# Performance work log

Hardware: AMD Instinct MI355X
Metric: run time of the kernel (lower is better)

## Reference

```python
import jax, jax.numpy as jnp
import numpy as np

K_SIZE = 5  # kernel_size


def _patches(f, k):
    # f: (b, c, h, w) -> (b, c, k*k, h, w), matching torch.nn.Unfold ordering
    # (patch positions row-major (kh, kw) per channel), padding = k//2, stride 1.
    p = k // 2
    b, c, h, w = f.shape
    fp = jnp.pad(f, ((0, 0), (0, 0), (p, p), (p, p)))
    slices = [fp[:, :, i:i + h, j:j + w] for i in range(k) for j in range(k)]
    return jnp.stack(slices, axis=2)


def _conv1x1(w, b, f):
    # w: (out, in), b: (out,), f: (b, in, h, w)
    return jnp.einsum('oc,bchw->bohw', w, f) + b[None, :, None, None]


def setup_inputs() -> dict:
    key = jax.random.key(0)
    ks = jax.random.split(key, 8)
    B, XC, YC, FT, H, W = 4, 64, 64, 64, 128, 128
    x = jax.random.normal(ks[0], (B, XC, H, W), dtype=jnp.float32)
    y = jax.random.normal(ks[1], (B, YC, H, W), dtype=jnp.float32)
    sx = 1.0 / np.sqrt(XC)
    sy = 1.0 / np.sqrt(YC)
    sf = 1.0 / np.sqrt(FT)
    wx = jax.random.uniform(ks[2], (FT, XC), jnp.float32, -sx, sx)
    bx = jax.random.uniform(ks[3], (FT,), jnp.float32, -sx, sx)
    wy = jax.random.uniform(ks[4], (FT, YC), jnp.float32, -sy, sy)
    by = jax.random.uniform(ks[5], (FT,), jnp.float32, -sy, sy)
    wo = jax.random.uniform(ks[6], (XC, FT), jnp.float32, -sf, sf)
    bo = jax.random.uniform(ks[7], (XC,), jnp.float32, -sf, sf)
    return {"x": x, "y": y, "wx": wx, "bx": bx, "wy": wy, "by": by, "wo": wo, "bo": bo}


def reference(x, y, wx, bx, wy, by, wo, bo):
    k = K_SIZE
    q = _conv1x1(wy, by, y)            # (b, feat, h, w): Q (the q axis of size 1 is squeezed)
    Kp = _patches(q, k)                # (b, feat, k^2, h, w): unfold(conv_y(y))
    v = _conv1x1(wx, bx, x)            # (b, feat, h, w)
    Vp = _patches(v, k)                # (b, feat, k^2, h, w): unfold(conv_x(x))
    A = jnp.einsum('bckhw,bchw->bkhw', Kp, q)   # scores over k^2 neighbors
    A = jax.nn.softmax(A, axis=1)               # softmax over dim=1 (k^2)
    out = jnp.einsum('bkhw,bckhw->bchw', A, Vp)  # aggregate values
    out = _conv1x1(wo, bo, out)
    return out + x
```

## Files before the change

### kernel.cpp

```cpp
#include <hip/hip_runtime.h>

#define HH   128
#define WW   128
#define HW   (HH * WW)
#define CC   64
#define BB   4
#define TILE 8
#define HALO 12

typedef unsigned int uint32;
typedef _Float16 h2  __attribute__((ext_vector_type(2)));
typedef __fp16   h2b __attribute__((ext_vector_type(2)));

__device__ __forceinline__ uint32 pkrtz(float a, float b) {
    h2b r = __builtin_amdgcn_cvt_pkrtz(a, b);
    return __builtin_bit_cast(uint32, r);
}
__device__ __forceinline__ float dot2(uint32 a, uint32 b, float c) {
#if __has_builtin(__builtin_amdgcn_fdot2)
    return __builtin_amdgcn_fdot2(__builtin_bit_cast(h2b, a),
                                  __builtin_bit_cast(h2b, b), c, false);
#else
    h2 x = __builtin_bit_cast(h2, a), y = __builtin_bit_cast(h2, b);
    return c + (float)x.x * (float)y.x + (float)x.y * (float)y.y;
#endif
}

__global__ __launch_bounds__(256, 4)
void qv_kernel(const float* __restrict__ x, const float* __restrict__ y,
               const float* __restrict__ wx, const float* __restrict__ bx,
               const float* __restrict__ wy, const float* __restrict__ by,
               uint32* __restrict__ qws, uint32* __restrict__ vws)
{
    __shared__ uint32 yP[32 * 64];
    __shared__ uint32 xP[32 * 64];
    __shared__ uint32 wyP[32 * 64];
    __shared__ uint32 wxP[32 * 64];

    const int t  = threadIdx.x;
    const int w0 = blockIdx.x * 64;
    const int h  = blockIdx.y;
    const int b  = blockIdx.z;

    {
        const int px = t & 63;
        const size_t rb = (size_t)b * CC * HW + (size_t)h * WW + w0 + px;
        #pragma unroll
        for (int i = 0; i < 8; ++i) {
            const int icp = (t >> 6) * 8 + i;
            const float y0 = y[rb + (size_t)(2 * icp) * HW];
            const float y1 = y[rb + (size_t)(2 * icp + 1) * HW];
            const float x0 = x[rb + (size_t)(2 * icp) * HW];
            const float x1 = x[rb + (size_t)(2 * icp + 1) * HW];
            yP[icp * 64 + px] = pkrtz(y0, y1);
            xP[icp * 64 + px] = pkrtz(x0, x1);
        }
        const int oc = t & 63;
        #pragma unroll
        for (int i = 0; i < 8; ++i) {
            const int icp = (t >> 6) * 8 + i;
            wyP[icp * 64 + oc] = pkrtz(wy[oc * CC + 2 * icp], wy[oc * CC + 2 * icp + 1]);
            wxP[icp * 64 + oc] = pkrtz(wx[oc * CC + 2 * icp], wx[oc * CC + 2 * icp + 1]);
        }
    }
    __syncthreads();

    const int oc0 = (t & 15) * 4;
    const int px0 = (t >> 4) * 4;

    float aq[4][4] = {{0.f}}, av[4][4] = {{0.f}};
    #pragma unroll 8
    for (int icp = 0; icp < 32; ++icp) {
        const uint4 yv = *(const uint4*)&yP[icp * 64 + px0];
        const uint4 xv = *(const uint4*)&xP[icp * 64 + px0];
        const uint4 wq = *(const uint4*)&wyP[icp * 64 + oc0];
        const uint4 wv = *(const uint4*)&wxP[icp * 64 + oc0];
        const uint32 yf[4] = {yv.x, yv.y, yv.z, yv.w};
        const uint32 xf[4] = {xv.x, xv.y, xv.z, xv.w};
        const uint32 wqf[4] = {wq.x, wq.y, wq.z, wq.w};
        const uint32 wvf[4] = {wv.x, wv.y, wv.z, wv.w};
        #pragma unroll
        for (int i = 0; i < 4; ++i)
            #pragma unroll
            for (int j = 0; j < 4; ++j) {
                aq[i][j] = dot2(wqf[i], yf[j], aq[i][j]);
                av[i][j] = dot2(wvf[i], xf[j], av[i][j]);
            }
    }

    float byf[4], bxf[4];
    #pragma unroll
    for (int i = 0; i < 4; ++i) { byf[i] = by[oc0 + i]; bxf[i] = bx[oc0 + i]; }
    const size_t ob = ((size_t)(b * HH + h) * WW + w0) * 32;
    #pragma unroll
    for (int j = 0; j < 4; ++j) {
        uint2 qo, vo;
        qo.x = pkrtz(aq[0][j] + byf[0], aq[1][j] + byf[1]);
        qo.y = pkrtz(aq[2][j] + byf[2], aq[3][j] + byf[3]);
        vo.x = pkrtz(av[0][j] + bxf[0], av[1][j] + bxf[1]);
        vo.y = pkrtz(av[2][j] + bxf[2], av[3][j] + bxf[3]);
        const size_t a = ob + (size_t)(px0 + j) * 32 + (oc0 >> 1);
        *(uint2*)&qws[a] = qo;
        *(uint2*)&vws[a] = vo;
    }
}

__global__ __launch_bounds__(256, 4)
void attn_kernel(const uint32* __restrict__ qws, const uint32* __restrict__ vws,
                 const float* __restrict__ x, const float* __restrict__ wo,
                 const float* __restrict__ bo, float* __restrict__ out)
{
    __shared__ uint32 qh[HALO * HALO * 32];
    __shared__ uint32 vh[HALO * HALO * 32];

    const int t   = threadIdx.x;
    const int b   = blockIdx.z;
    const int ty0 = blockIdx.y * TILE;
    const int tx0 = blockIdx.x * TILE;

    uint32 wpre[8];
    #pragma unroll
    for (int n = 0; n < 8; ++n) {
        const int k = n * 256 + t;
        const int oc = k >> 5, icp = k & 31;
        wpre[n] = pkrtz(wo[oc * CC + 2 * icp], wo[oc * CC + 2 * icp + 1]);
    }

    for (int i = t; i < HALO * HALO * 8; i += 256) {
        const int pix  = i >> 3, part = i & 7;
        const int phys = part ^ (pix & 7);
        const int hy   = pix / HALO;
        const int hx   = pix - hy * HALO;
        const int gy   = ty0 + hy - 2, gx = tx0 + hx - 2;
        uint4 q4 = {0u, 0u, 0u, 0u}, v4 = {0u, 0u, 0u, 0u};
        if ((unsigned)gy < HH && (unsigned)gx < WW) {
            const size_t a = ((size_t)(b * HH + gy) * WW + gx) * 32 + part * 4;
            q4 = *(const uint4*)(qws + a);
            v4 = *(const uint4*)(vws + a);
        }
        *(uint4*)&qh[pix * 32 + phys * 4] = q4;
        *(uint4*)&vh[pix * 32 + phys * 4] = v4;
    }
    __syncthreads();

    const int p    = t >> 2, sub = t & 3;
    const int py   = p >> 3, px  = p & 7;
    const int crow = (py + 2) * HALO + (px + 2);

    uint32 qc[8];
    {
        const int c0 = ((2 * sub) ^ (crow & 7)) * 4;
        const int c1 = ((2 * sub + 1) ^ (crow & 7)) * 4;
        *(uint4*)&qc[0] = *(const uint4*)&qh[crow * 32 + c0];
        *(uint4*)&qc[4] = *(const uint4*)&qh[crow * 32 + c1];
    }

    float sc[25];
    #pragma unroll
    for (int dy = 0; dy < 5; ++dy)
        #pragma unroll
        for (int dx = 0; dx < 5; ++dx) {
            const int nrow = (py + dy) * HALO + (px + dx);
            const int c0 = ((2 * sub) ^ (nrow & 7)) * 4;
            const int c1 = ((2 * sub + 1) ^ (nrow & 7)) * 4;
            const uint4 r0 = *(const uint4*)&qh[nrow * 32 + c0];
            const uint4 r1 = *(const uint4*)&qh[nrow * 32 + c1];
            float s = 0.f;
            s = dot2(qc[0], r0.x, s); s = dot2(qc[1], r0.y, s);
            s = dot2(qc[2], r0.z, s); s = dot2(qc[3], r0.w, s);
            s = dot2(qc[4], r1.x, s); s = dot2(qc[5], r1.y, s);
            s = dot2(qc[6], r1.z, s); s = dot2(qc[7], r1.w, s);
            s += __shfl_xor(s, 1);
            s += __shfl_xor(s, 2);
            sc[dy * 5 + dx] = s;
        }

    float mx = sc[0];
    #pragma unroll
    for (int k = 1; k < 25; ++k) mx = fmaxf(mx, sc[k]);
    float sum = 0.f;
    #pragma unroll
    for (int k = 0; k < 25; ++k) { sc[k] = __expf(sc[k] - mx); sum += sc[k]; }
    const float inv = 1.f / sum;

    h2 ag[8];
    #pragma unroll
    for (int k = 0; k < 8; ++k) ag[k] = (h2)(_Float16)0;
    #pragma unroll
    for (int dy = 0; dy < 5; ++dy)
        #pragma unroll
        for (int dx = 0; dx < 5; ++dx) {
            const int nrow = (py + dy) * HALO + (px + dx);
            const int c0 = ((2 * sub) ^ (nrow & 7)) * 4;
            const int c1 = ((2 * sub + 1) ^ (nrow & 7)) * 4;
            const uint4 r0 = *(const uint4*)&vh[nrow * 32 + c0];
            const uint4 r1 = *(const uint4*)&vh[nrow * 32 + c1];
            const _Float16 af = (_Float16)(sc[dy * 5 + dx] * inv);
            const h2 a2 = {af, af};
            ag[0] += a2 * __builtin_bit_cast(h2, r0.x);
            ag[1] += a2 * __builtin_bit_cast(h2, r0.y);
            ag[2] += a2 * __builtin_bit_cast(h2, r0.z);
            ag[3] += a2 * __builtin_bit_cast(h2, r0.w);
            ag[4] += a2 * __builtin_bit_cast(h2, r1.x);
            ag[5] += a2 * __builtin_bit_cast(h2, r1.y);
            ag[6] += a2 * __builtin_bit_cast(h2, r1.z);
            ag[7] += a2 * __builtin_bit_cast(h2, r1.w);
        }

    __syncthreads();
    {
        const int c0 = ((2 * sub) ^ (p & 7)) * 4;
        const int c1 = ((2 * sub + 1) ^ (p & 7)) * 4;
        uint4 w0, w1;
        w0.x = __builtin_bit_cast(uint32, ag[0]); w0.y = __builtin_bit_cast(uint32, ag[1]);
        w0.z = __builtin_bit_cast(uint32, ag[2]); w0.w = __builtin_bit_cast(uint32, ag[3]);
        w1.x = __builtin_bit_cast(uint32, ag[4]); w1.y = __builtin_bit_cast(uint32, ag[5]);
        w1.z = __builtin_bit_cast(uint32, ag[6]); w1.w = __builtin_bit_cast(uint32, ag[7]);
        *(uint4*)&qh[p * 32 + c0] = w0;
        *(uint4*)&qh[p * 32 + c1] = w1;
        #pragma unroll
        for (int n = 0; n < 8; ++n)
            qh[64 * 32 + n * 256 + t] = wpre[n];
    }
    __syncthreads();

    const int pp  = t & 63;
    const int ob2 = t >> 6;
    uint32 aggv[8 * 4];
    #pragma unroll
    for (int j = 0; j < 8; ++j)
        *(uint4*)&aggv[j * 4] = *(const uint4*)&qh[pp * 32 + (j ^ (pp & 7)) * 4];

    const int gh = ty0 + (pp >> 3), gw = tx0 + (pp & 7);
    #pragma unroll
    for (int o = 0; o < 16; ++o) {
        const int oc = ob2 * 16 + o;
        float acc = bo[oc];
        const uint32* wrow = &qh[(64 + oc) * 32];
        #pragma unroll
        for (int k = 0; k < 32; ++k) acc = dot2(aggv[k], wrow[k], acc);
        const size_t a = ((size_t)(b * CC + oc) * HH + gh) * WW + gw;
        out[a] = acc + x[a];
    }
}

extern "C" void kernel_launch(void* const* d_in, const int* in_sizes, int n_in,
                              void* d_out, int out_size, void* d_ws, size_t ws_size,
                              hipStream_t stream) {
    const float* x  = (const float*)d_in[0];
    const float* y  = (const float*)d_in[1];
    const float* wx = (const float*)d_in[2];
    const float* bx = (const float*)d_in[3];
    const float* wy = (const float*)d_in[4];
    const float* by = (const float*)d_in[5];
    const float* wo = (const float*)d_in[6];
    const float* bo = (const float*)d_in[7];
    float* out = (float*)d_out;

    uint32* qws = (uint32*)d_ws;
    uint32* vws = qws + (size_t)BB * HW * 32;

    dim3 gA(WW / 64, HH, BB);
    qv_kernel<<<gA, 256, 0, stream>>>(x, y, wx, bx, wy, by, qws, vws);

    dim3 gB(WW / TILE, HH / TILE, BB);
    attn_kernel<<<gB, 256, 0, stream>>>(qws, vws, x, wo, bo, out);
}
```

Baseline: 133.8 us.

## Fuse QV projection into attention kernel with MFMA 1x1 convolutions over halo

```diff
diff --git a/kernel.cpp b/kernel.cpp
--- a/kernel.cpp
+++ b/kernel.cpp
@@ -4,13 +4,15 @@
 #define WW   128
 #define HW   (HH * WW)
 #define CC   64
-#define BB   4
 #define TILE 8
 #define HALO 12
+#define NHP  (HALO * HALO)
 
 typedef unsigned int uint32;
-typedef _Float16 h2  __attribute__((ext_vector_type(2)));
-typedef __fp16   h2b __attribute__((ext_vector_type(2)));
+typedef _Float16 h2   __attribute__((ext_vector_type(2)));
+typedef __fp16   h2b  __attribute__((ext_vector_type(2)));
+typedef _Float16 h8   __attribute__((ext_vector_type(8)));
+typedef float    f32x4 __attribute__((ext_vector_type(4)));
 
 __device__ __forceinline__ uint32 pkrtz(float a, float b) {
     h2b r = __builtin_amdgcn_cvt_pkrtz(a, b);
@@ -25,127 +27,131 @@
     return c + (float)x.x * (float)y.x + (float)x.y * (float)y.y;
 #endif
 }
+__device__ __forceinline__ f32x4 mfma16(uint4 a, uint4 b, f32x4 c) {
+    return __builtin_amdgcn_mfma_f32_16x16x32_f16(
+        __builtin_bit_cast(h8, a), __builtin_bit_cast(h8, b), c, 0, 0, 0);
+}
+__device__ __forceinline__ uint4 pack_w8(const float* __restrict__ w) {
+    const float4 lo = *(const float4*)w;
+    const float4 hi = *(const float4*)(w + 4);
+    uint4 r;
+    r.x = pkrtz(lo.x, lo.y); r.y = pkrtz(lo.z, lo.w);
+    r.z = pkrtz(hi.x, hi.y); r.w = pkrtz(hi.z, hi.w);
+    return r;
+}
 
 __global__ __launch_bounds__(256, 4)
-void qv_kernel(const float* __restrict__ x, const float* __restrict__ y,
-               const float* __restrict__ wx, const float* __restrict__ bx,
-               const float* __restrict__ wy, const float* __restrict__ by,
-               uint32* __restrict__ qws, uint32* __restrict__ vws)
+void fused_attn(const float* __restrict__ x, const float* __restrict__ y,
+                const float* __restrict__ wx, const float* __restrict__ bx,
+                const float* __restrict__ wy, const float* __restrict__ by,
+                const float* __restrict__ wo, const float* __restrict__ bo,
+                float* __restrict__ out)
 {
-    __shared__ uint32 yP[32 * 64];
-    __shared__ uint32 xP[32 * 64];
-    __shared__ uint32 wyP[32 * 64];
-    __shared__ uint32 wxP[32 * 64];
-
-    const int t  = threadIdx.x;
-    const int w0 = blockIdx.x * 64;
-    const int h  = blockIdx.y;
-    const int b  = blockIdx.z;
-
-    {
-        const int px = t & 63;
-        const size_t rb = (size_t)b * CC * HW + (size_t)h * WW + w0 + px;
-        #pragma unroll
-        for (int i = 0; i < 8; ++i) {
-            const int icp = (t >> 6) * 8 + i;
-            const float y0 = y[rb + (size_t)(2 * icp) * HW];
-            const float y1 = y[rb + (size_t)(2 * icp + 1) * HW];
-            const float x0 = x[rb + (size_t)(2 * icp) * HW];
-            const float x1 = x[rb + (size_t)(2 * icp + 1) * HW];
-            yP[icp * 64 + px] = pkrtz(y0, y1);
-            xP[icp * 64 + px] = pkrtz(x0, x1);
-        }
-        const int oc = t & 63;
-        #pragma unroll
-        for (int i = 0; i < 8; ++i) {
-            const int icp = (t >> 6) * 8 + i;
-            wyP[icp * 64 + oc] = pkrtz(wy[oc * CC + 2 * icp], wy[oc * CC + 2 * icp + 1]);
-            wxP[icp * 64 + oc] = pkrtz(wx[oc * CC + 2 * icp], wx[oc * CC + 2 * icp + 1]);
-        }
-    }
-    __syncthreads();
-
-    const int oc0 = (t & 15) * 4;
-    const int px0 = (t >> 4) * 4;
-
-    float aq[4][4] = {{0.f}}, av[4][4] = {{0.f}};
-    #pragma unroll 8
-    for (int icp = 0; icp < 32; ++icp) {
-        const uint4 yv = *(const uint4*)&yP[icp * 64 + px0];
-        const uint4 xv = *(const uint4*)&xP[icp * 64 + px0];
-        const uint4 wq = *(const uint4*)&wyP[icp * 64 + oc0];
-        const uint4 wv = *(const uint4*)&wxP[icp * 64 + oc0];
-        const uint32 yf[4] = {yv.x, yv.y, yv.z, yv.w};
-        const uint32 xf[4] = {xv.x, xv.y, xv.z, xv.w};
-        const uint32 wqf[4] = {wq.x, wq.y, wq.z, wq.w};
-        const uint32 wvf[4] = {wv.x, wv.y, wv.z, wv.w};
-        #pragma unroll
-        for (int i = 0; i < 4; ++i)
-            #pragma unroll
-            for (int j = 0; j < 4; ++j) {
-                aq[i][j] = dot2(wqf[i], yf[j], aq[i][j]);
-                av[i][j] = dot2(wvf[i], xf[j], av[i][j]);
-            }
-    }
-
-    float byf[4], bxf[4];
-    #pragma unroll
-    for (int i = 0; i < 4; ++i) { byf[i] = by[oc0 + i]; bxf[i] = bx[oc0 + i]; }
-    const size_t ob = ((size_t)(b * HH + h) * WW + w0) * 32;
-    #pragma unroll
-    for (int j = 0; j < 4; ++j) {
-        uint2 qo, vo;
-        qo.x = pkrtz(aq[0][j] + byf[0], aq[1][j] + byf[1]);
-        qo.y = pkrtz(aq[2][j] + byf[2], aq[3][j] + byf[3]);
-        vo.x = pkrtz(av[0][j] + bxf[0], av[1][j] + bxf[1]);
-        vo.y = pkrtz(av[2][j] + bxf[2], av[3][j] + bxf[3]);
-        const size_t a = ob + (size_t)(px0 + j) * 32 + (oc0 >> 1);
-        *(uint2*)&qws[a] = qo;
-        *(uint2*)&vws[a] = vo;
-    }
-}
-
-__global__ __launch_bounds__(256, 4)
-void attn_kernel(const uint32* __restrict__ qws, const uint32* __restrict__ vws,
-                 const float* __restrict__ x, const float* __restrict__ wo,
-                 const float* __restrict__ bo, float* __restrict__ out)
-{
-    __shared__ uint32 qh[HALO * HALO * 32];
-    __shared__ uint32 vh[HALO * HALO * 32];
+    __shared__ uint32 qh[NHP * 32];
+    __shared__ uint32 vh[NHP * 32];
 
     const int t   = threadIdx.x;
     const int b   = blockIdx.z;
     const int ty0 = blockIdx.y * TILE;
     const int tx0 = blockIdx.x * TILE;
 
-    uint32 wpre[8];
-    #pragma unroll
-    for (int n = 0; n < 8; ++n) {
-        const int k = n * 256 + t;
-        const int oc = k >> 5, icp = k & 31;
-        wpre[n] = pkrtz(wo[oc * CC + 2 * icp], wo[oc * CC + 2 * icp + 1]);
-    }
-
-    for (int i = t; i < HALO * HALO * 8; i += 256) {
-        const int pix  = i >> 3, part = i & 7;
-        const int phys = part ^ (pix & 7);
-        const int hy   = pix / HALO;
-        const int hx   = pix - hy * HALO;
-        const int gy   = ty0 + hy - 2, gx = tx0 + hx - 2;
-        uint4 q4 = {0u, 0u, 0u, 0u}, v4 = {0u, 0u, 0u, 0u};
-        if ((unsigned)gy < HH && (unsigned)gx < WW) {
-            const size_t a = ((size_t)(b * HH + gy) * WW + gx) * 32 + part * 4;
-            q4 = *(const uint4*)(qws + a);
-            v4 = *(const uint4*)(vws + a);
-        }
-        *(uint4*)&qh[pix * 32 + phys * 4] = q4;
-        *(uint4*)&vh[pix * 32 + phys * 4] = v4;
+    for (int i = t; i < NHP * 8; i += 256) {
+        const int c   = i / NHP;
+        const int pix = i - c * NHP;
+        const int hy  = pix / HALO, hx = pix - hy * HALO;
+        int gy = ty0 + hy - 2, gx = tx0 + hx - 2;
+        const bool ok = ((unsigned)gy < HH) & ((unsigned)gx < WW);
+        if (!ok) { gy = 0; gx = 0; }
+        const size_t base = (size_t)b * CC * HW + (size_t)(c * 8) * HW
+                          + (size_t)gy * WW + gx;
+        float yv[8], xv[8];
+        #pragma unroll
+        for (int j = 0; j < 8; ++j) {
+            yv[j] = y[base + (size_t)j * HW];
+            xv[j] = x[base + (size_t)j * HW];
+        }
+        uint4 yq, xq;
+        yq.x = pkrtz(yv[0], yv[1]); yq.y = pkrtz(yv[2], yv[3]);
+        yq.z = pkrtz(yv[4], yv[5]); yq.w = pkrtz(yv[6], yv[7]);
+        xq.x = pkrtz(xv[0], xv[1]); xq.y = pkrtz(xv[2], xv[3]);
+        xq.z = pkrtz(xv[4], xv[5]); xq.w = pkrtz(xv[6], xv[7]);
+        const int w0 = (c ^ (pix & 7)) * 4;
+        *(uint4*)&qh[pix * 32 + w0] = yq;
+        *(uint4*)&vh[pix * 32 + w0] = xq;
+    }
+    __syncthreads();
+
+    const int wv = t >> 6;
+    const int ln = t & 63;
+    const int lm = ln & 15;
+    const int qd = ln >> 4;
+
+    {
+        const uint4 a0 = pack_w8(wy + (wv * 16 + lm) * CC + qd * 8);
+        const uint4 a1 = pack_w8(wy + (wv * 16 + lm) * CC + qd * 8 + 32);
+        f32x4 acc[9];
+        #pragma unroll
+        for (int nt = 0; nt < 9; ++nt) {
+            const int px = nt * 16 + lm, sw = px & 7;
+            const uint4 b0 = *(const uint4*)&qh[px * 32 + ((qd    ) ^ sw) * 4];
+            const uint4 b1 = *(const uint4*)&qh[px * 32 + ((qd + 4) ^ sw) * 4];
+            f32x4 a = {0.f, 0.f, 0.f, 0.f};
+            a = mfma16(a0, b0, a);
+            a = mfma16(a1, b1, a);
+            acc[nt] = a;
+        }
+        __syncthreads();
+        const float4 bq = *(const float4*)(by + wv * 16 + qd * 4);
+        const int chunk = wv * 2 + (qd >> 1);
+        #pragma unroll
+        for (int nt = 0; nt < 9; ++nt) {
+            const int px = nt * 16 + lm;
+            const int hy = px / HALO, hx = px - hy * HALO;
+            const int gy = ty0 + hy - 2, gx = tx0 + hx - 2;
+            uint2 wp = {0u, 0u};
+            if (((unsigned)gy < HH) & ((unsigned)gx < WW)) {
+                wp.x = pkrtz(acc[nt].x + bq.x, acc[nt].y + bq.y);
+                wp.y = pkrtz(acc[nt].z + bq.z, acc[nt].w + bq.w);
+            }
+            *(uint2*)&qh[px * 32 + (chunk ^ (px & 7)) * 4 + (qd & 1) * 2] = wp;
+        }
+    }
+
+    {
+        const uint4 a0 = pack_w8(wx + (wv * 16 + lm) * CC + qd * 8);
+        const uint4 a1 = pack_w8(wx + (wv * 16 + lm) * CC + qd * 8 + 32);
+        f32x4 acc[9];
+        #pragma unroll
+        for (int nt = 0; nt < 9; ++nt) {
+            const int px = nt * 16 + lm, sw = px & 7;
+            const uint4 b0 = *(const uint4*)&vh[px * 32 + ((qd    ) ^ sw) * 4];
+            const uint4 b1 = *(const uint4*)&vh[px * 32 + ((qd + 4) ^ sw) * 4];
+            f32x4 a = {0.f, 0.f, 0.f, 0.f};
+            a = mfma16(a0, b0, a);
+            a = mfma16(a1, b1, a);
+            acc[nt] = a;
+        }
+        __syncthreads();
+        const float4 bq = *(const float4*)(bx + wv * 16 + qd * 4);
+        const int chunk = wv * 2 + (qd >> 1);
+        #pragma unroll
+        for (int nt = 0; nt < 9; ++nt) {
+            const int px = nt * 16 + lm;
+            const int hy = px / HALO, hx = px - hy * HALO;
+            const int gy = ty0 + hy - 2, gx = tx0 + hx - 2;
+            uint2 wp = {0u, 0u};
+            if (((unsigned)gy < HH) & ((unsigned)gx < WW)) {
+                wp.x = pkrtz(acc[nt].x + bq.x, acc[nt].y + bq.y);
+                wp.y = pkrtz(acc[nt].z + bq.z, acc[nt].w + bq.w);
+            }
+            *(uint2*)&vh[px * 32 + (chunk ^ (px & 7)) * 4 + (qd & 1) * 2] = wp;
+        }
     }
     __syncthreads();
 
     const int p    = t >> 2, sub = t & 3;
-    const int py   = p >> 3, px  = p & 7;
-    const int crow = (py + 2) * HALO + (px + 2);
+    const int py   = p >> 3, px8 = p & 7;
+    const int crow = (py + 2) * HALO + (px8 + 2);
 
     uint32 qc[8];
     {
@@ -160,7 +166,7 @@
     for (int dy = 0; dy < 5; ++dy)
         #pragma unroll
         for (int dx = 0; dx < 5; ++dx) {
-            const int nrow = (py + dy) * HALO + (px + dx);
+            const int nrow = (py + dy) * HALO + (px8 + dx);
             const int c0 = ((2 * sub) ^ (nrow & 7)) * 4;
             const int c1 = ((2 * sub + 1) ^ (nrow & 7)) * 4;
             const uint4 r0 = *(const uint4*)&qh[nrow * 32 + c0];
@@ -190,7 +196,7 @@
     for (int dy = 0; dy < 5; ++dy)
         #pragma unroll
         for (int dx = 0; dx < 5; ++dx) {
-            const int nrow = (py + dy) * HALO + (px + dx);
+            const int nrow = (py + dy) * HALO + (px8 + dx);
             const int c0 = ((2 * sub) ^ (nrow & 7)) * 4;
             const int c1 = ((2 * sub + 1) ^ (nrow & 7)) * 4;
             const uint4 r0 = *(const uint4*)&vh[nrow * 32 + c0];
@@ -218,29 +224,30 @@
         w1.z = __builtin_bit_cast(uint32, ag[6]); w1.w = __builtin_bit_cast(uint32, ag[7]);
         *(uint4*)&qh[p * 32 + c0] = w0;
         *(uint4*)&qh[p * 32 + c1] = w1;
-        #pragma unroll
-        for (int n = 0; n < 8; ++n)
-            qh[64 * 32 + n * 256 + t] = wpre[n];
-    }
-    __syncthreads();
-
-    const int pp  = t & 63;
-    const int ob2 = t >> 6;
-    uint32 aggv[8 * 4];
-    #pragma unroll
-    for (int j = 0; j < 8; ++j)
-        *(uint4*)&aggv[j * 4] = *(const uint4*)&qh[pp * 32 + (j ^ (pp & 7)) * 4];
-
-    const int gh = ty0 + (pp >> 3), gw = tx0 + (pp & 7);
-    #pragma unroll
-    for (int o = 0; o < 16; ++o) {
-        const int oc = ob2 * 16 + o;
-        float acc = bo[oc];
-        const uint32* wrow = &qh[(64 + oc) * 32];
-        #pragma unroll
-        for (int k = 0; k < 32; ++k) acc = dot2(aggv[k], wrow[k], acc);
-        const size_t a = ((size_t)(b * CC + oc) * HH + gh) * WW + gw;
-        out[a] = acc + x[a];
+    }
+    __syncthreads();
+
+    {
+        const uint4 a0 = pack_w8(wo + (wv * 16 + lm) * CC + qd * 8);
+        const uint4 a1 = pack_w8(wo + (wv * 16 + lm) * CC + qd * 8 + 32);
+        const float4 bq = *(const float4*)(bo + wv * 16 + qd * 4);
+        #pragma unroll
+        for (int nt = 0; nt < 4; ++nt) {
+            const int px = nt * 16 + lm, sw = px & 7;
+            const uint4 b0 = *(const uint4*)&qh[px * 32 + ((qd    ) ^ sw) * 4];
+            const uint4 b1 = *(const uint4*)&qh[px * 32 + ((qd + 4) ^ sw) * 4];
+            f32x4 a = {0.f, 0.f, 0.f, 0.f};
+            a = mfma16(a0, b0, a);
+            a = mfma16(a1, b1, a);
+            const int gh = ty0 + (px >> 3), gw = tx0 + (px & 7);
+            const float av4[4] = {a.x + bq.x, a.y + bq.y, a.z + bq.z, a.w + bq.w};
+            #pragma unroll
+            for (int r = 0; r < 4; ++r) {
+                const int oc = wv * 16 + qd * 4 + r;
+                const size_t ad = (size_t)(b * CC + oc) * HW + (size_t)gh * WW + gw;
+                out[ad] = av4[r] + x[ad];
+            }
+        }
     }
 }
 
@@ -256,13 +263,8 @@
     const float* wo = (const float*)d_in[6];
     const float* bo = (const float*)d_in[7];
     float* out = (float*)d_out;
-
-    uint32* qws = (uint32*)d_ws;
-    uint32* vws = qws + (size_t)BB * HW * 32;
-
-    dim3 gA(WW / 64, HH, BB);
-    qv_kernel<<<gA, 256, 0, stream>>>(x, y, wx, bx, wy, by, qws, vws);
-
-    dim3 gB(WW / TILE, HH / TILE, BB);
-    attn_kernel<<<gB, 256, 0, stream>>>(qws, vws, x, wo, bo, out);
-}
+    (void)d_ws; (void)ws_size;
+
+    dim3 grid(WW / TILE, HH / TILE, 4);
+    fused_attn<<<grid, 256, 0, stream>>>(x, y, wx, bx, wy, by, wo, bo, out);
+}
```

New measurement: 136.7 us. 1.02x slower.
